# Kernel tuning notes

Hardware: AMD Instinct MI355X
Metric: run time of the kernel (lower is better)

Reference implementation:

```python
import jax, jax.numpy as jnp
import numpy as np

EPS = 1e-8


def setup_inputs() -> dict:
    key = jax.random.key(0)
    ks = jax.random.split(key, 8)
    B, N, D = 8, 1024, 256
    x = jax.random.normal(ks[0], (B, N, D), dtype=jnp.float32)
    y = jax.random.normal(ks[1], (B, N, D), dtype=jnp.float32)
    coords = jax.random.normal(ks[2], (N, N, 6), dtype=jnp.float32)
    # xavier-ish init for U, kaiming-ish for S1/S2
    U = jax.random.normal(ks[3], (D, D), dtype=jnp.float32) * (1.0 / np.sqrt(D))
    S1 = jax.random.normal(ks[4], (D, 1), dtype=jnp.float32)
    S2 = jax.random.normal(ks[5], (D, 1), dtype=jnp.float32)
    gating = jnp.asarray(1.0, dtype=jnp.float32)
    h_temp = jnp.asarray(0.1, dtype=jnp.float32)
    p_temp = jnp.asarray(1.0, dtype=jnp.float32)
    # trunc_normal_(a=0, b=1): std-normal truncated to [0, 1]
    pos_emb = jax.random.truncated_normal(ks[6], 0.0, 1.0, (N, 6, 1)).astype(jnp.float32)
    return {"x": x, "y": y, "coords": coords, "U": U, "S1": S1, "S2": S2,
            "gating": gating, "h_temp": h_temp, "p_temp": p_temp, "pos_emb": pos_emb}


def _spectral(x, U, S):
    # x @ U.T @ diag(|S|) @ U  ==  ((x @ U.T) * |S|) @ U
    s = jnp.abs(S[:, 0])
    return ((x @ U.T) * s) @ U


def reference(x, y, coords, U, S1, S2, gating, h_temp, p_temp, pos_emb):
    B, N, D = x.shape
    scale = D ** (-0.5)
    xs = jnp.stack([_spectral(x, U, S1), _spectral(x, U, S2)], axis=1)  # [B,2,N,D]
    # patch attention scores: [B,2,N,N]
    patch_score = jax.nn.softmax(jnp.einsum('bknd,bmd->bknm', xs, y) * scale, axis=-1)
    # positional scores, shared across batch and the 2 spectral branches: [N,N]
    pos_logits = -jnp.abs(p_temp) * jnp.einsum('nmc,ncq->nm', coords, pos_emb)
    pos_score = jax.nn.softmax(pos_logits, axis=-1)
    g = jax.nn.sigmoid(gating)
    attn = (1.0 - g) * patch_score + g * pos_score[None, None]  # [B,2,N,N]
    # entropy over key axis -> [B,N,2]
    entropy = jnp.sum(-attn * jnp.log(attn + EPS), axis=-1).transpose(0, 2, 1)
    hmap = 2.0 - 2.0 * jax.nn.sigmoid(h_temp * entropy)  # [B,N,2]
    fgbg = hmap[..., 0] >= hmap[..., 1]
    route = jax.lax.stop_gradient(
        jnp.stack([fgbg, ~fgbg], axis=-1).astype(hmap.dtype))  # [B,N,2]
    heat_map = jnp.sum(hmap * route, axis=-1, keepdims=True)  # [B,N,1]
    attn_sel = jnp.sum(attn * route.transpose(0, 2, 1)[..., None], axis=1)  # [B,N,N]
    out = attn_sel @ y  # [B,N,D]
    return (out, heat_map)
```

## Files before the change

kernel.cpp:

```cpp
#include <hip/hip_runtime.h>
#include <hip/hip_bf16.h>
#include <stdint.h>


#define NB 8
#define NN_ 1024
#define ND 256

typedef __bf16 bf16x8 __attribute__((ext_vector_type(8)));
typedef __bf16 bf16x4 __attribute__((ext_vector_type(4)));
typedef float f32x4 __attribute__((ext_vector_type(4)));

__device__ inline void gl_lds(const __bf16* g, __bf16* l) {
    auto gp = (const __attribute__((address_space(1))) uint32_t*)(uintptr_t)g;
    auto lp = (__attribute__((address_space(3))) uint32_t*)(uintptr_t)l;
    __builtin_amdgcn_global_load_lds(gp, lp, 16, 0, 0);
}

__device__ inline float wred_sum(float v) {
#pragma unroll
    for (int o = 32; o; o >>= 1) v += __shfl_xor(v, o, 64);
    return v;
}
__device__ inline float wred_max(float v) {
#pragma unroll
    for (int o = 32; o; o >>= 1) v = fmaxf(v, __shfl_xor(v, o, 64));
    return v;
}

__global__ __launch_bounds__(256) void prep_kernel(
    const float* __restrict__ coords, const float* __restrict__ pos_emb,
    const float* __restrict__ p_temp, const float* __restrict__ x,
    const float* __restrict__ y, const float* __restrict__ U,
    const float* __restrict__ S1, const float* __restrict__ S2,
    float* __restrict__ posS, __bf16* __restrict__ Xh, __bf16* __restrict__ Xl,
    __bf16* __restrict__ yt, __bf16* __restrict__ Yh, __bf16* __restrict__ Yl,
    __bf16* __restrict__ Mh, __bf16* __restrict__ Ml) {
    __shared__ char sm[9216 + 64];
    const int bid = blockIdx.x;
    const int tid = threadIdx.x;

    if (bid < 1024) {
        float* red = (float*)sm;
        const int n = bid;
        const float pt = -fabsf(p_temp[0]);
        float pe[6];
#pragma unroll
        for (int c = 0; c < 6; ++c) pe[c] = pos_emb[n * 6 + c];
        const float* cr = coords + (long)n * NN_ * 6;
        float l[4];
#pragma unroll
        for (int j = 0; j < 4; ++j) {
            const int m = j * 256 + tid;
            const float2* cp = (const float2*)(cr + (long)m * 6);
            float2 c0 = cp[0], c1 = cp[1], c2 = cp[2];
            l[j] = pt * (c0.x * pe[0] + c0.y * pe[1] + c1.x * pe[2] +
                         c1.y * pe[3] + c2.x * pe[4] + c2.y * pe[5]);
        }
        float mx = fmaxf(fmaxf(l[0], l[1]), fmaxf(l[2], l[3]));
        mx = wred_max(mx);
        __syncthreads();
        if ((tid & 63) == 0) red[tid >> 6] = mx;
        __syncthreads();
        mx = fmaxf(fmaxf(red[0], red[1]), fmaxf(red[2], red[3]));
        float e[4], s = 0.f;
#pragma unroll
        for (int j = 0; j < 4; ++j) { e[j] = __expf(l[j] - mx); s += e[j]; }
        s = wred_sum(s);
        __syncthreads();
        if ((tid & 63) == 0) red[4 + (tid >> 6)] = s;
        __syncthreads();
        s = red[4] + red[5] + red[6] + red[7];
        const float inv = 1.f / s;
#pragma unroll
        for (int j = 0; j < 4; ++j)
            posS[(long)n * NN_ + j * 256 + tid] = e[j] * inv;
    } else if (bid < 1536) {
        const int n4 = NB * NN_ * ND / 4;
        int i = (bid - 1024) * 256 + tid;
        for (; i < n4; i += 512 * 256) {
            float4 v = ((const float4*)x)[i];
            bf16x4 h, l;
            h[0] = (__bf16)v.x; l[0] = (__bf16)(v.x - (float)h[0]);
            h[1] = (__bf16)v.y; l[1] = (__bf16)(v.y - (float)h[1]);
            h[2] = (__bf16)v.z; l[2] = (__bf16)(v.z - (float)h[2]);
            h[3] = (__bf16)v.w; l[3] = (__bf16)(v.w - (float)h[3]);
            ((bf16x4*)Xh)[i] = h;
            ((bf16x4*)Xl)[i] = l;
        }
    } else if (bid < 2048) {
        __bf16 (*t)[72] = (__bf16(*)[72])sm;
        const int rem = bid - 1536;
        const int b = rem >> 6;
        const int m0 = (rem & 15) * 64, d0 = ((rem >> 4) & 3) * 64;
        const int c = tid & 15;
        const int r = tid >> 4;
#pragma unroll
        for (int p = 0; p < 4; ++p) {
            const int row = r + p * 16;
            const long gi = ((long)b * NN_ + m0 + row) * ND + d0 + c * 4;
            float4 v = *(const float4*)(y + gi);
            bf16x4 h, l;
            h[0] = (__bf16)v.x; l[0] = (__bf16)(v.x - (float)h[0]);
            h[1] = (__bf16)v.y; l[1] = (__bf16)(v.y - (float)h[1]);
            h[2] = (__bf16)v.z; l[2] = (__bf16)(v.z - (float)h[2]);
            h[3] = (__bf16)v.w; l[3] = (__bf16)(v.w - (float)h[3]);
            *(bf16x4*)(Yh + gi) = h;
            *(bf16x4*)(Yl + gi) = l;
            t[c * 4 + 0][row] = h[0]; t[c * 4 + 1][row] = h[1];
            t[c * 4 + 2][row] = h[2]; t[c * 4 + 3][row] = h[3];
        }
        __syncthreads();
#pragma unroll
        for (int p = 0; p < 4; ++p) {
            const int d = r + p * 16;
            bf16x4 o;
            o[0] = t[d][c * 4 + 0]; o[1] = t[d][c * 4 + 1];
            o[2] = t[d][c * 4 + 2]; o[3] = t[d][c * 4 + 3];
            *(bf16x4*)(yt + ((long)b * ND + d0 + d) * NN_ + m0 + c * 4) = o;
        }
    } else {
        const int n = bid - 2048, j = tid;
        float a1 = 0.f, a2 = 0.f;
        for (int c = 0; c < ND; ++c) {
            const float un = U[c * ND + n];
            const float uj = U[c * ND + j];
            a1 = fmaf(fabsf(S1[c]) * un, uj, a1);
            a2 = fmaf(fabsf(S2[c]) * un, uj, a2);
        }
        const __bf16 h1 = (__bf16)a1, h2 = (__bf16)a2;
        Mh[n * ND + j] = h1;           Ml[n * ND + j] = (__bf16)(a1 - (float)h1);
        Mh[65536 + n * ND + j] = h2;   Ml[65536 + n * ND + j] = (__bf16)(a2 - (float)h2);
    }
}

__global__ __launch_bounds__(256) void mgemm_xs(
    const __bf16* __restrict__ Ah, const __bf16* __restrict__ Al,
    const __bf16* __restrict__ Bh, const __bf16* __restrict__ Bl,
    __bf16* __restrict__ Ch, __bf16* __restrict__ Cl,
    int M, int N, int K, long sB1, long sC) {
    constexpr int BM = 128, BK = 32, BN = 64;
    __shared__ __bf16 As[2 * BM * BK];
    __shared__ __bf16 Bs[2 * BN * BK];

    const int z = blockIdx.z;
    Bh += (long)z * sB1; Bl += (long)z * sB1;

    const int tid = threadIdx.x;
    const int bm = blockIdx.y * BM, bn = blockIdx.x * BN;
    const int wave = tid >> 6, lane = tid & 63;
    const int wm = wave >> 1, wn = wave & 1;
    const int quad = lane >> 4, l16 = lane & 15;

    f32x4 acc[4][2];
#pragma unroll
    for (int i = 0; i < 4; ++i)
#pragma unroll
        for (int j = 0; j < 2; ++j) acc[i][j] = (f32x4){0.f, 0.f, 0.f, 0.f};

    const int srow = lane >> 2;
    const int slot = lane & 3;

    for (int k0 = 0; k0 < K; k0 += BK) {
        __syncthreads();
#pragma unroll
        for (int i = 0; i < 2; ++i) {
            const int r0 = wave * 32 + i * 16;
            const int row = r0 + srow;
            const int chunk = slot ^ ((row >> 1) & 3);
            const long g = (long)(bm + row) * K + k0 + chunk * 8;
            gl_lds(Ah + g, &As[r0 * 32]);
            gl_lds(Al + g, &As[BM * BK + r0 * 32]);
        }
        {
            const int r0 = wave * 16;
            const int row = r0 + srow;
            const int chunk = slot ^ ((row >> 1) & 3);
            const long g = (long)(bn + row) * K + k0 + chunk * 8;
            gl_lds(Bh + g, &Bs[r0 * 32]);
            gl_lds(Bl + g, &Bs[BN * BK + r0 * 32]);
        }
        __syncthreads();

        bf16x8 a_h[4], a_l[4], b_h[2], b_l[2];
#pragma unroll
        for (int mi = 0; mi < 4; ++mi) {
            const int row = wm * 64 + mi * 16 + l16;
            const int off = row * 32 + ((quad ^ ((row >> 1) & 3)) * 8);
            a_h[mi] = *(const bf16x8*)&As[off];
            a_l[mi] = *(const bf16x8*)&As[BM * BK + off];
        }
#pragma unroll
        for (int ni = 0; ni < 2; ++ni) {
            const int row = wn * 32 + ni * 16 + l16;
            const int off = row * 32 + ((quad ^ ((row >> 1) & 3)) * 8);
            b_h[ni] = *(const bf16x8*)&Bs[off];
            b_l[ni] = *(const bf16x8*)&Bs[BN * BK + off];
        }
#pragma unroll
        for (int mi = 0; mi < 4; ++mi)
#pragma unroll
            for (int ni = 0; ni < 2; ++ni) {
                acc[mi][ni] = __builtin_amdgcn_mfma_f32_16x16x32_bf16(
                    a_h[mi], b_h[ni], acc[mi][ni], 0, 0, 0);
                acc[mi][ni] = __builtin_amdgcn_mfma_f32_16x16x32_bf16(
                    a_h[mi], b_l[ni], acc[mi][ni], 0, 0, 0);
                acc[mi][ni] = __builtin_amdgcn_mfma_f32_16x16x32_bf16(
                    a_l[mi], b_h[ni], acc[mi][ni], 0, 0, 0);
            }
    }

    Ch += (long)z * sC; Cl += (long)z * sC;
#pragma unroll
    for (int mi = 0; mi < 4; ++mi) {
        const int row0 = bm + wm * 64 + mi * 16 + quad * 4;
#pragma unroll
        for (int ni = 0; ni < 2; ++ni) {
            const int col = bn + wn * 32 + ni * 16 + l16;
#pragma unroll
            for (int r = 0; r < 4; ++r) {
                const float v = acc[mi][ni][r];
                const long idx = (long)(row0 + r) * N + col;
                const __bf16 h = (__bf16)v;
                Ch[idx] = h;
                Cl[idx] = (__bf16)(v - (float)h);
            }
        }
    }
}

__global__ __launch_bounds__(256) void mgemm_sc(
    const __bf16* __restrict__ Ah, const __bf16* __restrict__ Al,
    const __bf16* __restrict__ Bh, const __bf16* __restrict__ Bl,
    float* __restrict__ C, int N, int K,
    long sA1, long sA2, long sB1, long sC, float alpha) {
    constexpr int BM = 128, BK = 32, BN = 128;
    __shared__ __bf16 As[2 * BM * BK];
    __shared__ __bf16 Bs[2 * BN * BK];

    const int bid = blockIdx.x;
    const int xcd = bid & 7;
    const int j   = bid >> 3;
    const int z   = 2 * xcd + (j >> 6);
    const int t   = j & 63;
    const int bm  = (t >> 3) * BM;
    const int bn  = (t & 7) * BN;

    const long aoff = (long)(z >> 1) * sA1 + (long)(z & 1) * sA2;
    const long boff = (long)(z >> 1) * sB1;
    Ah += aoff; Al += aoff;
    Bh += boff; Bl += boff;

    const int tid = threadIdx.x;
    const int wave = tid >> 6, lane = tid & 63;
    const int wm = wave >> 1, wn = wave & 1;
    const int quad = lane >> 4, l16 = lane & 15;

    f32x4 acc[4][4];
#pragma unroll
    for (int i = 0; i < 4; ++i)
#pragma unroll
        for (int jj = 0; jj < 4; ++jj) acc[i][jj] = (f32x4){0.f, 0.f, 0.f, 0.f};

    const int srow = lane >> 2;
    const int slot = lane & 3;

    for (int k0 = 0; k0 < K; k0 += BK) {
        __syncthreads();
#pragma unroll
        for (int i = 0; i < 2; ++i) {
            const int r0 = wave * 32 + i * 16;
            const int row = r0 + srow;
            const int chunk = slot ^ ((row >> 1) & 3);
            const long ga = (long)(bm + row) * K + k0 + chunk * 8;
            gl_lds(Ah + ga, &As[r0 * 32]);
            gl_lds(Al + ga, &As[BM * BK + r0 * 32]);
            const long gb = (long)(bn + row) * K + k0 + chunk * 8;
            gl_lds(Bh + gb, &Bs[r0 * 32]);
            gl_lds(Bl + gb, &Bs[BN * BK + r0 * 32]);
        }
        __syncthreads();

        bf16x8 a_h[4], a_l[4], b_h[4], b_l[4];
#pragma unroll
        for (int mi = 0; mi < 4; ++mi) {
            const int row = wm * 64 + mi * 16 + l16;
            const int off = row * 32 + ((quad ^ ((row >> 1) & 3)) * 8);
            a_h[mi] = *(const bf16x8*)&As[off];
            a_l[mi] = *(const bf16x8*)&As[BM * BK + off];
        }
#pragma unroll
        for (int ni = 0; ni < 4; ++ni) {
            const int row = wn * 64 + ni * 16 + l16;
            const int off = row * 32 + ((quad ^ ((row >> 1) & 3)) * 8);
            b_h[ni] = *(const bf16x8*)&Bs[off];
            b_l[ni] = *(const bf16x8*)&Bs[BN * BK + off];
        }
#pragma unroll
        for (int mi = 0; mi < 4; ++mi)
#pragma unroll
            for (int ni = 0; ni < 4; ++ni) {
                acc[mi][ni] = __builtin_amdgcn_mfma_f32_16x16x32_bf16(
                    a_h[mi], b_h[ni], acc[mi][ni], 0, 0, 0);
                acc[mi][ni] = __builtin_amdgcn_mfma_f32_16x16x32_bf16(
                    a_h[mi], b_l[ni], acc[mi][ni], 0, 0, 0);
                acc[mi][ni] = __builtin_amdgcn_mfma_f32_16x16x32_bf16(
                    a_l[mi], b_h[ni], acc[mi][ni], 0, 0, 0);
            }
    }

    C += (long)z * sC;
#pragma unroll
    for (int mi = 0; mi < 4; ++mi) {
        const int row0 = bm + wm * 64 + mi * 16 + quad * 4;
#pragma unroll
        for (int ni = 0; ni < 4; ++ni) {
            const int col = bn + wn * 64 + ni * 16 + l16;
#pragma unroll
            for (int r = 0; r < 4; ++r)
                C[(long)(row0 + r) * NN_ + col] = acc[mi][ni][r] * alpha;
        }
    }
}

__global__ __launch_bounds__(256, 8) void blendsm_kernel(
    const float* __restrict__ S, const float* __restrict__ pos,
    const float* __restrict__ gating, const float* __restrict__ h_temp,
    __bf16* __restrict__ P, float* __restrict__ heat) {
    const int b = blockIdx.x & 7;
    const int n = (blockIdx.x >> 3) * 4 + (threadIdx.x >> 6);
    const int lane = threadIdx.x & 63;

    const float g = 1.f / (1.f + __expf(-gating[0]));
    const float cg = 1.f - g;
    const float ht = h_temp[0];

    const float* r0p = S + ((long)(b * 2 + 0) * NN_ + n) * NN_;
    const float* r1p = S + ((long)(b * 2 + 1) * NN_ + n) * NN_;

    f32x4 a0[4], a1[4];
#pragma unroll
    for (int j = 0; j < 4; ++j) {
        a0[j] = *(const f32x4*)(r0p + j * 256 + lane * 4);
        a1[j] = *(const f32x4*)(r1p + j * 256 + lane * 4);
    }
    float m0 = -3.4e38f, m1 = -3.4e38f;
#pragma unroll
    for (int j = 0; j < 4; ++j) {
        m0 = fmaxf(m0, fmaxf(fmaxf(a0[j][0], a0[j][1]), fmaxf(a0[j][2], a0[j][3])));
        m1 = fmaxf(m1, fmaxf(fmaxf(a1[j][0], a1[j][1]), fmaxf(a1[j][2], a1[j][3])));
    }
    m0 = wred_max(m0); m1 = wred_max(m1);
    float s0 = 0.f, s1 = 0.f;
#pragma unroll
    for (int j = 0; j < 4; ++j) {
        a0[j][0] = __expf(a0[j][0] - m0); a0[j][1] = __expf(a0[j][1] - m0);
        a0[j][2] = __expf(a0[j][2] - m0); a0[j][3] = __expf(a0[j][3] - m0);
        s0 += a0[j][0] + a0[j][1] + a0[j][2] + a0[j][3];
        a1[j][0] = __expf(a1[j][0] - m1); a1[j][1] = __expf(a1[j][1] - m1);
        a1[j][2] = __expf(a1[j][2] - m1); a1[j][3] = __expf(a1[j][3] - m1);
        s1 += a1[j][0] + a1[j][1] + a1[j][2] + a1[j][3];
    }
    s0 = wred_sum(s0); s1 = wred_sum(s1);
    const float i0 = 1.f / s0, i1 = 1.f / s1;
    const float* pr = pos + (long)n * NN_;
    float e0 = 0.f, e1 = 0.f;
#pragma unroll
    for (int j = 0; j < 4; ++j) {
        const f32x4 pv = *(const f32x4*)(pr + j * 256 + lane * 4);
        a0[j][0] = cg * a0[j][0] * i0 + g * pv[0];
        a0[j][1] = cg * a0[j][1] * i0 + g * pv[1];
        a0[j][2] = cg * a0[j][2] * i0 + g * pv[2];
        a0[j][3] = cg * a0[j][3] * i0 + g * pv[3];
        a1[j][0] = cg * a1[j][0] * i1 + g * pv[0];
        a1[j][1] = cg * a1[j][1] * i1 + g * pv[1];
        a1[j][2] = cg * a1[j][2] * i1 + g * pv[2];
        a1[j][3] = cg * a1[j][3] * i1 + g * pv[3];
        e0 -= a0[j][0] * __logf(a0[j][0] + 1e-8f) + a0[j][1] * __logf(a0[j][1] + 1e-8f) +
              a0[j][2] * __logf(a0[j][2] + 1e-8f) + a0[j][3] * __logf(a0[j][3] + 1e-8f);
        e1 -= a1[j][0] * __logf(a1[j][0] + 1e-8f) + a1[j][1] * __logf(a1[j][1] + 1e-8f) +
              a1[j][2] * __logf(a1[j][2] + 1e-8f) + a1[j][3] * __logf(a1[j][3] + 1e-8f);
    }
    e0 = wred_sum(e0); e1 = wred_sum(e1);
    const float hm0 = 2.f - 2.f / (1.f + __expf(-ht * e0));
    const float hm1 = 2.f - 2.f / (1.f + __expf(-ht * e1));
    const bool fg = (hm0 >= hm1);
    if (lane == 0) heat[(long)b * NN_ + n] = fg ? hm0 : hm1;
    __bf16* prow = P + ((long)b * NN_ + n) * NN_;
#pragma unroll
    for (int j = 0; j < 4; ++j) {
        const f32x4 v = fg ? a0[j] : a1[j];
        bf16x4 o;
        o[0] = (__bf16)v[0]; o[1] = (__bf16)v[1];
        o[2] = (__bf16)v[2]; o[3] = (__bf16)v[3];
        *(bf16x4*)(prow + j * 256 + lane * 4) = o;
    }
}

__global__ __launch_bounds__(256) void pv_gemm(
    const __bf16* __restrict__ A, const __bf16* __restrict__ Bm,
    float* __restrict__ C) {
    constexpr int BM = 32, BK = 32, BN = 64;
    __shared__ __bf16 As[2][BM * BK];
    __shared__ __bf16 Bs[2][BN * BK];

    const int bid = blockIdx.x;
    const int b   = bid & 7;
    const int j   = bid >> 3;
    const int bm  = (j >> 2) * BM;
    const int bn  = (j & 3) * BN;

    A  += (long)b * NN_ * NN_;
    Bm += (long)b * ND * NN_;
    C  += (long)b * NN_ * ND;

    const int tid = threadIdx.x;
    const int wave = tid >> 6, lane = tid & 63;
    const int wm = wave >> 1, wn = wave & 1;
    const int quad = lane >> 4, l16 = lane & 15;
    const int srow = lane >> 2, slot = lane & 3;

    f32x4 acc[2];
    acc[0] = (f32x4){0.f, 0.f, 0.f, 0.f};
    acc[1] = (f32x4){0.f, 0.f, 0.f, 0.f};

    auto stage = [&](int sel, int k0) {
        if (wave < 2) {
            const int row = wave * 16 + srow;
            const int chunk = slot ^ ((row >> 1) & 3);
            gl_lds(A + (long)(bm + row) * NN_ + k0 + chunk * 8,
                   &As[sel][wave * 16 * 32]);
        }
        {
            const int row = wave * 16 + srow;
            const int chunk = slot ^ ((row >> 1) & 3);
            gl_lds(Bm + (long)(bn + row) * NN_ + k0 + chunk * 8,
                   &Bs[sel][wave * 16 * 32]);
        }
    };

    stage(0, 0);
    __syncthreads();
    int cur = 0;
    for (int k0 = 0; k0 < NN_; k0 += BK) {
        if (k0 + BK < NN_) stage(cur ^ 1, k0 + BK);

        const int arow = wm * 16 + l16;
        const int aoff = arow * 32 + ((quad ^ ((arow >> 1) & 3)) * 8);
        bf16x8 a = *(const bf16x8*)&As[cur][aoff];
#pragma unroll
        for (int ni = 0; ni < 2; ++ni) {
            const int brow = wn * 32 + ni * 16 + l16;
            const int boff = brow * 32 + ((quad ^ ((brow >> 1) & 3)) * 8);
            bf16x8 bb = *(const bf16x8*)&Bs[cur][boff];
            acc[ni] = __builtin_amdgcn_mfma_f32_16x16x32_bf16(
                a, bb, acc[ni], 0, 0, 0);
        }

        __syncthreads();
        cur ^= 1;
    }

    const int row0 = bm + wm * 16 + quad * 4;
#pragma unroll
    for (int ni = 0; ni < 2; ++ni) {
        const int col = bn + wn * 32 + ni * 16 + l16;
#pragma unroll
        for (int r = 0; r < 4; ++r)
            C[(long)(row0 + r) * ND + col] = acc[ni][r];
    }
}

extern "C" void kernel_launch(void* const* d_in, const int* in_sizes, int n_in,
                              void* d_out, int out_size, void* d_ws, size_t ws_size,
                              hipStream_t stream) {
    const float* x      = (const float*)d_in[0];
    const float* y      = (const float*)d_in[1];
    const float* coords = (const float*)d_in[2];
    const float* U      = (const float*)d_in[3];
    const float* S1p    = (const float*)d_in[4];
    const float* S2p    = (const float*)d_in[5];
    const float* gating = (const float*)d_in[6];
    const float* h_temp = (const float*)d_in[7];
    const float* p_temp = (const float*)d_in[8];
    const float* pos_emb= (const float*)d_in[9];

    float* out  = (float*)d_out;
    float* heat = out + (long)NB * NN_ * ND;

    char* ws = (char*)d_ws;
    const long MB = 1 << 20;
    float*  Sf  = (float*)(ws);
    float*  pos = (float*)(ws + 64 * MB);
    __bf16* Xh  = (__bf16*)(ws + 68 * MB);
    __bf16* Xl  = (__bf16*)(ws + 72 * MB);
    __bf16* XSh = (__bf16*)(ws + 76 * MB);
    __bf16* XSl = (__bf16*)(ws + 84 * MB);
    __bf16* yt  = (__bf16*)(ws + 92 * MB);
    __bf16* Yh  = (__bf16*)(ws + 96 * MB);
    __bf16* Yl  = (__bf16*)(ws + 100 * MB);
    __bf16* Mh  = (__bf16*)(ws + 104 * MB);
    __bf16* Ml  = Mh + 2 * 65536;
    __bf16* Pb  = (__bf16*)(ws + 76 * MB);

    const long ND2 = (long)NN_ * ND;
    const long BND = (long)NB * ND2;

    prep_kernel<<<dim3(2304), 256, 0, stream>>>(
        coords, pos_emb, p_temp, x, y, U, S1p, S2p,
        pos, Xh, Xl, yt, Yh, Yl, Mh, Ml);

    mgemm_xs<<<dim3(4, 64, 2), 256, 0, stream>>>(
        Xh, Xl, Mh, Ml, XSh, XSl, NB * NN_, ND, ND, 65536, BND);

    mgemm_sc<<<dim3(1024), 256, 0, stream>>>(
        XSh, XSl, Yh, Yl, Sf, NN_, ND,
        ND2, BND, ND2, (long)NN_ * NN_, 0.0625f);

    blendsm_kernel<<<dim3(2048), 256, 0, stream>>>(
        Sf, pos, gating, h_temp, Pb, heat);

    pv_gemm<<<dim3(1024), 256, 0, stream>>>(Pb, yt, out);

    (void)in_sizes; (void)n_in; (void)out_size; (void)ws_size;
}
```

Measured before the change: 202.6 us.

## Double-buffer LDS in spectral GEMM and halve M tile for more blocks

The xs GEMM now double-buffers its shared-memory tiles, issuing the global-to-LDS loads for the next K step before computing on the current one and keeping one barrier per iteration. The M tile shrinks from 128 to 64, which doubles the grid to 1024 blocks for better CU occupancy and cuts per-thread accumulators. The aim is to hide load latency and fill the GPU better on a small GEMM, at the cost of less reuse of B tiles and more total global traffic.

```diff
diff --git a/kernel.cpp b/kernel.cpp
--- a/kernel.cpp
+++ b/kernel.cpp
@@ -139,9 +139,9 @@
     const __bf16* __restrict__ Bh, const __bf16* __restrict__ Bl,
     __bf16* __restrict__ Ch, __bf16* __restrict__ Cl,
     int M, int N, int K, long sB1, long sC) {
-    constexpr int BM = 128, BK = 32, BN = 64;
-    __shared__ __bf16 As[2 * BM * BK];
-    __shared__ __bf16 Bs[2 * BN * BK];
+    constexpr int BM = 64, BK = 32, BN = 64;
+    __shared__ __bf16 As[2][2 * BM * BK];
+    __shared__ __bf16 Bs[2][2 * BN * BK];
 
     const int z = blockIdx.z;
     Bh += (long)z * sB1; Bl += (long)z * sB1;
@@ -151,54 +151,49 @@
     const int wave = tid >> 6, lane = tid & 63;
     const int wm = wave >> 1, wn = wave & 1;
     const int quad = lane >> 4, l16 = lane & 15;
-
-    f32x4 acc[4][2];
-#pragma unroll
-    for (int i = 0; i < 4; ++i)
+    const int srow = lane >> 2, slot = lane & 3;
+
+    f32x4 acc[2][2];
+#pragma unroll
+    for (int i = 0; i < 2; ++i)
 #pragma unroll
         for (int j = 0; j < 2; ++j) acc[i][j] = (f32x4){0.f, 0.f, 0.f, 0.f};
 
-    const int srow = lane >> 2;
-    const int slot = lane & 3;
-
+    auto stage = [&](int sel, int k0) {
+        const int r0 = wave * 16;
+        const int row = r0 + srow;
+        const int chunk = slot ^ ((row >> 1) & 3);
+        const long ga = (long)(bm + row) * K + k0 + chunk * 8;
+        gl_lds(Ah + ga, &As[sel][r0 * 32]);
+        gl_lds(Al + ga, &As[sel][BM * BK + r0 * 32]);
+        const long gb = (long)(bn + row) * K + k0 + chunk * 8;
+        gl_lds(Bh + gb, &Bs[sel][r0 * 32]);
+        gl_lds(Bl + gb, &Bs[sel][BN * BK + r0 * 32]);
+    };
+
+    stage(0, 0);
+    __syncthreads();
+    int cur = 0;
     for (int k0 = 0; k0 < K; k0 += BK) {
-        __syncthreads();
-#pragma unroll
-        for (int i = 0; i < 2; ++i) {
-            const int r0 = wave * 32 + i * 16;
-            const int row = r0 + srow;
-            const int chunk = slot ^ ((row >> 1) & 3);
-            const long g = (long)(bm + row) * K + k0 + chunk * 8;
-            gl_lds(Ah + g, &As[r0 * 32]);
-            gl_lds(Al + g, &As[BM * BK + r0 * 32]);
-        }
-        {
-            const int r0 = wave * 16;
-            const int row = r0 + srow;
-            const int chunk = slot ^ ((row >> 1) & 3);
-            const long g = (long)(bn + row) * K + k0 + chunk * 8;
-            gl_lds(Bh + g, &Bs[r0 * 32]);
-            gl_lds(Bl + g, &Bs[BN * BK + r0 * 32]);
-        }
-        __syncthreads();
-
-        bf16x8 a_h[4], a_l[4], b_h[2], b_l[2];
-#pragma unroll
-        for (int mi = 0; mi < 4; ++mi) {
-            const int row = wm * 64 + mi * 16 + l16;
+        if (k0 + BK < K) stage(cur ^ 1, k0 + BK);
+
+        bf16x8 a_h[2], a_l[2], b_h[2], b_l[2];
+#pragma unroll
+        for (int mi = 0; mi < 2; ++mi) {
+            const int row = wm * 32 + mi * 16 + l16;
             const int off = row * 32 + ((quad ^ ((row >> 1) & 3)) * 8);
-            a_h[mi] = *(const bf16x8*)&As[off];
-            a_l[mi] = *(const bf16x8*)&As[BM * BK + off];
+            a_h[mi] = *(const bf16x8*)&As[cur][off];
+            a_l[mi] = *(const bf16x8*)&As[cur][BM * BK + off];
         }
 #pragma unroll
         for (int ni = 0; ni < 2; ++ni) {
             const int row = wn * 32 + ni * 16 + l16;
             const int off = row * 32 + ((quad ^ ((row >> 1) & 3)) * 8);
-            b_h[ni] = *(const bf16x8*)&Bs[off];
-            b_l[ni] = *(const bf16x8*)&Bs[BN * BK + off];
-        }
-#pragma unroll
-        for (int mi = 0; mi < 4; ++mi)
+            b_h[ni] = *(const bf16x8*)&Bs[cur][off];
+            b_l[ni] = *(const bf16x8*)&Bs[cur][BN * BK + off];
+        }
+#pragma unroll
+        for (int mi = 0; mi < 2; ++mi)
 #pragma unroll
             for (int ni = 0; ni < 2; ++ni) {
                 acc[mi][ni] = __builtin_amdgcn_mfma_f32_16x16x32_bf16(
@@ -208,12 +203,15 @@
                 acc[mi][ni] = __builtin_amdgcn_mfma_f32_16x16x32_bf16(
                     a_l[mi], b_h[ni], acc[mi][ni], 0, 0, 0);
             }
+
+        __syncthreads();
+        cur ^= 1;
     }
 
     Ch += (long)z * sC; Cl += (long)z * sC;
 #pragma unroll
-    for (int mi = 0; mi < 4; ++mi) {
-        const int row0 = bm + wm * 64 + mi * 16 + quad * 4;
+    for (int mi = 0; mi < 2; ++mi) {
+        const int row0 = bm + wm * 32 + mi * 16 + quad * 4;
 #pragma unroll
         for (int ni = 0; ni < 2; ++ni) {
             const int col = bn + wn * 32 + ni * 16 + l16;
@@ -510,7 +508,7 @@
         coords, pos_emb, p_temp, x, y, U, S1p, S2p,
         pos, Xh, Xl, yt, Yh, Yl, Mh, Ml);
 
-    mgemm_xs<<<dim3(4, 64, 2), 256, 0, stream>>>(
+    mgemm_xs<<<dim3(4, 128, 2), 256, 0, stream>>>(
         Xh, Xl, Mh, Ml, XSh, XSl, NB * NN_, ND, ND, 65536, BND);
 
     mgemm_sc<<<dim3(1024), 256, 0, stream>>>(
```

Measured after the change: 196.4 us. -3.1%, faster.
